# Optimization experiments

Measured on AMD Instinct MI355X. Metric: run time of the kernel, lower is better.

The kernel has to match this reference:

```python
import jax, jax.numpy as jnp
import numpy as np

EMBED_DIM = 1024
EPS = 1e-6


def setup_inputs() -> dict:
    key = jax.random.key(0)
    ks = jax.random.split(key, 9)
    L, B, E = 2048, 4, EMBED_DIM
    s = 1.0 / np.sqrt(E)
    return {
        "query": jax.random.normal(ks[0], (L, B, E), jnp.float32),
        "key": jax.random.normal(ks[1], (L, B, E), jnp.float32),
        "value": jax.random.normal(ks[2], (L, B, E), jnp.float32),
        "Wq": jax.random.normal(ks[3], (E, E), jnp.float32) * s,
        "bq": jnp.zeros((E,), jnp.float32),
        "Wk": jax.random.normal(ks[4], (E, E), jnp.float32) * s,
        "bk": jnp.zeros((E,), jnp.float32),
        "Wv": jax.random.normal(ks[5], (E, E), jnp.float32) * s,
        "bv": jnp.zeros((E,), jnp.float32),
    }


def reference(query, key, value, Wq, bq, Wk, bk, Wv, bv):
    # query: (L, B, E); key/value: (S, B, E)
    L, B, E = query.shape
    S = key.shape[0]
    m = max(L, S)  # static

    # projections + relu feature map, then (B, T, E) layout
    q = jax.nn.relu(jnp.einsum("lbe,fe->lbf", query, Wq) + bq).transpose(1, 0, 2)
    k = jax.nn.relu(jnp.einsum("sbe,fe->sbf", key, Wk) + bk).transpose(1, 0, 2)
    v = (jnp.einsum("sbe,fe->sbf", value, Wv) + bv).transpose(1, 0, 2)

    # cosFormer positional weights: (pi/2) * (i+1) / m, i in [0, T)
    half_pi = jnp.float32(np.pi / 2)
    q_idx = (half_pi * jnp.arange(1, L + 1, dtype=jnp.float32) / m)[None, :, None]
    k_idx = (half_pi * jnp.arange(1, S + 1, dtype=jnp.float32) / m)[None, :, None]

    q_ = jnp.concatenate([q * jnp.sin(q_idx), q * jnp.cos(q_idx)], axis=-1)  # (B, L, 2E)
    k_ = jnp.concatenate([k * jnp.sin(k_idx), k * jnp.cos(k_idx)], axis=-1)  # (B, S, 2E)

    # linear attention: kv_ state (B, E, 2E), normalizer z_ (B, L)
    kv_ = jnp.einsum("nsd,nsm->nmd", k_, v)
    z_ = 1.0 / jnp.maximum(jnp.einsum("nld,nd->nl", q_, k_.sum(axis=1)), EPS)
    attn = jnp.einsum("nld,nmd,nl->nlm", q_, kv_, z_)  # (B, L, E)
    return attn.transpose(1, 0, 2)  # (L, B, E)
```

## Files before the change

kernel.cpp:

```cpp
#include <hip/hip_runtime.h>
#include <hip/hip_fp16.h>


typedef _Float16 f16;
typedef f16 f16x8 __attribute__((ext_vector_type(8)));
typedef f16 f16x4 __attribute__((ext_vector_type(4)));
typedef float f32x4 __attribute__((ext_vector_type(4)));

#define AS1 __attribute__((address_space(1)))
#define AS3 __attribute__((address_space(3)))

__device__ __forceinline__ void gload_lds16(const void* g, void* l) {
  __builtin_amdgcn_global_load_lds((const AS1 void*)g, (AS3 void*)l, 16, 0, 0);
}

__device__ __forceinline__ void xcd_swz(int& bx, int& by, int& bz) {
  const int nx = gridDim.x, ny = gridDim.y;
  const int p = blockIdx.x + nx * (blockIdx.y + ny * blockIdx.z);
  const int chunk = (nx * ny * gridDim.z) >> 3;
  const int l = (p & 7) * chunk + (p >> 3);
  bx = l % nx;
  by = (l / nx) % ny;
  bz = l / (nx * ny);
}

__global__ void cvt3(const float* __restrict__ s0, const float* __restrict__ s1,
                     const float* __restrict__ s2, f16* __restrict__ d0,
                     f16* __restrict__ d1, f16* __restrict__ d2, int n4) {
  const int z = blockIdx.z;
  const float* s = (z == 0) ? s0 : (z == 1) ? s1 : s2;
  f16* d = (z == 0) ? d0 : (z == 1) ? d1 : d2;
  const int i = blockIdx.x * 256 + threadIdx.x;
  if (i >= n4) return;
  const float4 v = ((const float4*)s)[i];
  f16x4 o = { (f16)v.x, (f16)v.y, (f16)v.z, (f16)v.w };
  ((f16x4*)d)[i] = o;
}

__device__ __forceinline__ void mm_core(const f16* __restrict__ A, int lda,
                                        const f16* __restrict__ B, int ldb,
                                        int K, int m0, int n0,
                                        f16* As0, f16* Bs0, f16* As1, f16* Bs1,
                                        f16* As2, f16* Bs2, f16* As3, f16* Bs3,
                                        f32x4 (&acc)[4][4]) {
  const int tid  = threadIdx.x;
  const int lane = tid & 63;
  const int w    = tid >> 6;
  const int wm   = w >> 1, wn = w & 1;
  const int l15  = lane & 15;
  const int quad = lane >> 4;

  const f16* pa0 = A + (long)(m0 + w * 16 + l15) * lda + quad * 8;
  const f16* pa1 = A + (long)(m0 + (8 + w) * 16 + l15) * lda + quad * 8;
  const f16* pb0 = B + (long)(n0 + w * 16 + l15) * ldb + quad * 8;
  int koff = 0;

#define STAGE_(Ab, Bb) do {                        \
    gload_lds16(pa0 + koff, (Ab) + w * 512);       \
    gload_lds16(pa1 + koff, (Ab) + (8 + w) * 512); \
    gload_lds16(pb0 + koff, (Bb) + w * 512);       \
    koff += 32; } while (0)

#define COMPUTE_(Ab, Bb) do {                                                    \
    f16x8 af[4], bf[4];                                                          \
    _Pragma("unroll")                                                            \
    for (int i = 0; i < 4; ++i)                                                  \
      af[i] = *(const f16x8*)((Ab) + (wm * 4 + i) * 512 + lane * 8);             \
    _Pragma("unroll")                                                            \
    for (int j = 0; j < 4; ++j)                                                  \
      bf[j] = *(const f16x8*)((Bb) + (wn * 4 + j) * 512 + lane * 8);             \
    _Pragma("unroll")                                                            \
    for (int i = 0; i < 4; ++i)                                                  \
      _Pragma("unroll")                                                          \
      for (int j = 0; j < 4; ++j)                                                \
        acc[i][j] = __builtin_amdgcn_mfma_f32_16x16x32_f16(af[i], bf[j],         \
                                                           acc[i][j], 0, 0, 0); \
  } while (0)

#define WV3_ asm volatile("s_waitcnt vmcnt(3)" ::: "memory")
#define WV0_ asm volatile("s_waitcnt vmcnt(0)" ::: "memory")
#define BARR_ do { __builtin_amdgcn_s_barrier(); __builtin_amdgcn_sched_barrier(0); } while (0)

  STAGE_(As0, Bs0);
  STAGE_(As1, Bs1);

  const int nt = K >> 5;
  for (int t = 0; t + 5 < nt; t += 4) {
    WV3_; BARR_; STAGE_(As2, Bs2); COMPUTE_(As0, Bs0);
    WV3_; BARR_; STAGE_(As3, Bs3); COMPUTE_(As1, Bs1);
    WV3_; BARR_; STAGE_(As0, Bs0); COMPUTE_(As2, Bs2);
    WV3_; BARR_; STAGE_(As1, Bs1); COMPUTE_(As3, Bs3);
  }
  WV3_; BARR_; STAGE_(As2, Bs2); COMPUTE_(As0, Bs0);
  WV3_; BARR_; STAGE_(As3, Bs3); COMPUTE_(As1, Bs1);
  WV3_; BARR_; COMPUTE_(As2, Bs2);
  WV0_; BARR_; COMPUTE_(As3, Bs3);

#undef STAGE_
#undef COMPUTE_
#undef WV3_
#undef WV0_
#undef BARR_
}

#define GEMM_LDS                                   \
  __shared__ alignas(16) f16 As0[8192];            \
  __shared__ alignas(16) f16 Bs0[4096];            \
  __shared__ alignas(16) f16 As1[8192];            \
  __shared__ alignas(16) f16 Bs1[4096];            \
  __shared__ alignas(16) f16 As2[8192];            \
  __shared__ alignas(16) f16 Bs2[4096];            \
  __shared__ alignas(16) f16 As3[8192];            \
  __shared__ alignas(16) f16 Bs3[4096];

__launch_bounds__(512, 2)
__global__ void proj_gemm(const f16* __restrict__ q16, const f16* __restrict__ k16,
                          const f16* __restrict__ v16, const f16* __restrict__ wq,
                          const f16* __restrict__ wk, const f16* __restrict__ wv,
                          const float* __restrict__ bq, const float* __restrict__ bk,
                          const float* __restrict__ bv,
                          f16* __restrict__ Qf, f16* __restrict__ Kn, f16* __restrict__ Vp) {
  GEMM_LDS
  int bx, by, z;
  xcd_swz(bx, by, z);
  const f16* A = (z == 0) ? q16 : (z == 1) ? k16 : v16;
  const f16* B = (z == 0) ? wq : (z == 1) ? wk : wv;
  const float* bias = (z == 0) ? bq : (z == 1) ? bk : bv;
  const int m0 = by * 256;
  const int n0 = bx * 128;

  f32x4 acc[4][4] = {};
  mm_core(A, 1024, B, 1024, 1024, m0, n0,
          As0, Bs0, As1, Bs1, As2, Bs2, As3, Bs3, acc);

  const int tid  = threadIdx.x;
  const int lane = tid & 63;
  const int w    = tid >> 6;
  const int wm   = w >> 1, wn = w & 1;
  const int l15  = lane & 15;
  const int quad = lane >> 4;

  if (z < 2) {
    f16* C = (z == 0) ? Qf : Kn;
    const int ldc = 2048, halfw = 1024;
#pragma unroll
    for (int i = 0; i < 4; ++i) {
      const int mg = m0 + wm * 64 + i * 16 + quad * 4;
      float sn[4], cn[4];
#pragma unroll
      for (int rr = 0; rr < 4; ++rr) {
        const int l = (mg + rr) >> 2;
        const float ang = 7.6699039394282066e-4f * (float)(l + 1);
        __sincosf(ang, &sn[rr], &cn[rr]);
      }
#pragma unroll
      for (int j = 0; j < 4; ++j) {
        const int ng = n0 + wn * 64 + j * 16 + l15;
        const float bc = bias[ng];
#pragma unroll
        for (int rr = 0; rr < 4; ++rr) {
          const float v = fmaxf(acc[i][j][rr] + bc, 0.f);
          C[(long)(mg + rr) * ldc + ng]         = (f16)(v * sn[rr]);
          C[(long)(mg + rr) * ldc + ng + halfw] = (f16)(v * cn[rr]);
        }
      }
    }
  } else {
    f16* C = Vp;
    const int ldc = 1024;
#pragma unroll
    for (int i = 0; i < 4; ++i) {
      const int mg = m0 + wm * 64 + i * 16 + quad * 4;
#pragma unroll
      for (int j = 0; j < 4; ++j) {
        const int ng = n0 + wn * 64 + j * 16 + l15;
        const float bc = bias[ng];
#pragma unroll
        for (int rr = 0; rr < 4; ++rr)
          C[(long)(mg + rr) * ldc + ng] = (f16)(acc[i][j][rr] + bc);
      }
    }
  }
}

template<int MODE>
__launch_bounds__(512, 2)
__global__ void gemm_bt(const f16* __restrict__ A, int lda,
                        const f16* __restrict__ B, int ldb,
                        void* __restrict__ Cout, int K, int ldc,
                        const float* __restrict__ zvec,
                        long abatch, long bbatch, long cbatch)
{
  GEMM_LDS
  int bx, by, bz;
  xcd_swz(bx, by, bz);
  A += (long)bz * abatch;
  B += (long)bz * bbatch;
  const int m0 = by * 256;
  const int n0 = bx * 128;

  f32x4 acc[4][4] = {};
  mm_core(A, lda, B, ldb, K, m0, n0,
          As0, Bs0, As1, Bs1, As2, Bs2, As3, Bs3, acc);

  const int tid  = threadIdx.x;
  const int lane = tid & 63;
  const int w    = tid >> 6;
  const int wm   = w >> 1, wn = w & 1;
  const int l15  = lane & 15;
  const int quad = lane >> 4;

  if constexpr (MODE == 2) {
    f16* C = (f16*)Cout + (long)bz * cbatch;
#pragma unroll
    for (int i = 0; i < 4; ++i) {
      const int mg = m0 + wm * 64 + i * 16 + quad * 4;
#pragma unroll
      for (int j = 0; j < 4; ++j) {
        const int ng = n0 + wn * 64 + j * 16 + l15;
#pragma unroll
        for (int rr = 0; rr < 4; ++rr)
          C[(long)(mg + rr) * ldc + ng] = (f16)acc[i][j][rr];
      }
    }
  } else {
    float* C = (float*)Cout + (long)bz * cbatch;
#pragma unroll
    for (int i = 0; i < 4; ++i) {
      const int mg = m0 + wm * 64 + i * 16 + quad * 4;
      float zr[4];
#pragma unroll
      for (int rr = 0; rr < 4; ++rr) zr[rr] = zvec[(long)(mg + rr) * 4 + bz];
#pragma unroll
      for (int j = 0; j < 4; ++j) {
        const int ng = n0 + wn * 64 + j * 16 + l15;
#pragma unroll
        for (int rr = 0; rr < 4; ++rr)
          C[(long)(mg + rr) * ldc + ng] = acc[i][j][rr] * zr[rr];
      }
    }
  }
}

__global__ void transpose_fused(const f16* __restrict__ Kn, f16* __restrict__ Kt,
                                const f16* __restrict__ Vp, f16* __restrict__ Vt) {
  __shared__ f16 tile[64 * 72];
  const int z = blockIdx.z;
  const f16* in;
  f16* out;
  long in_batch, out_batch;
  int ldin, ldout, b;
  if (z < 4) {
    in = Kn; out = Kt; in_batch = 2048; out_batch = 2048L * 2048;
    ldin = 8192; ldout = 2048; b = z;
  } else {
    if (blockIdx.x >= 16) return;
    in = Vp; out = Vt; in_batch = 1024; out_batch = 1024L * 2048;
    ldin = 4096; ldout = 2048; b = z - 4;
  }
  in  += (long)b * in_batch;
  out += (long)b * out_batch;
  const int r0 = blockIdx.y * 64;
  const int c0 = blockIdx.x * 64;
  const int t  = threadIdx.x;
  {
    const int r = t >> 2, cs = (t & 3) * 16;
    const f16* src = in + (long)(r0 + r) * ldin + c0 + cs;
    f16x8 v0 = *(const f16x8*)(src);
    f16x8 v1 = *(const f16x8*)(src + 8);
    *(f16x8*)(tile + r * 72 + cs)     = v0;
    *(f16x8*)(tile + r * 72 + cs + 8) = v1;
  }
  __syncthreads();
  {
    const int c = t >> 2, rs = (t & 3) * 16;
    alignas(16) f16 tmp[16];
#pragma unroll
    for (int j = 0; j < 16; ++j) tmp[j] = tile[(rs + j) * 72 + c];
    f16* dst = out + (long)(c0 + c) * ldout + r0 + rs;
    *(f16x8*)(dst)     = *(const f16x8*)(tmp);
    *(f16x8*)(dst + 8) = *(const f16x8*)(tmp + 8);
  }
}

__global__ void ksum_kernel(const f16* __restrict__ Kt, float* __restrict__ ks) {
  const long row = blockIdx.x;
  const int t = threadIdx.x;
  f16x8 v = *(const f16x8*)(Kt + row * 2048 + t * 8);
  float s = 0.f;
#pragma unroll
  for (int j = 0; j < 8; ++j) s += (float)v[j];
#pragma unroll
  for (int off = 32; off > 0; off >>= 1) s += __shfl_down(s, off, 64);
  __shared__ float red[4];
  if ((t & 63) == 0) red[t >> 6] = s;
  __syncthreads();
  if (t == 0) ks[row] = red[0] + red[1] + red[2] + red[3];
}

__global__ void z_kernel(const f16* __restrict__ Qf, const float* __restrict__ ks,
                         float* __restrict__ zb) {
  const long r = blockIdx.x;
  const int t = threadIdx.x;
  const int b = (int)(r & 3);
  f16x8 q = *(const f16x8*)(Qf + r * 2048 + t * 8);
  const float* kp = ks + b * 2048 + t * 8;
  float s = 0.f;
#pragma unroll
  for (int j = 0; j < 8; ++j) s += (float)q[j] * kp[j];
#pragma unroll
  for (int off = 32; off > 0; off >>= 1) s += __shfl_down(s, off, 64);
  __shared__ float red[4];
  if ((t & 63) == 0) red[t >> 6] = s;
  __syncthreads();
  if (t == 0) zb[r] = 1.f / fmaxf(red[0] + red[1] + red[2] + red[3], 1e-6f);
}

extern "C" void kernel_launch(void* const* d_in, const int* in_sizes, int n_in,
                              void* d_out, int out_size, void* d_ws, size_t ws_size,
                              hipStream_t stream) {
  const float* query = (const float*)d_in[0];
  const float* key_  = (const float*)d_in[1];
  const float* value = (const float*)d_in[2];
  const float* Wq    = (const float*)d_in[3];
  const float* bq    = (const float*)d_in[4];
  const float* Wk    = (const float*)d_in[5];
  const float* bk    = (const float*)d_in[6];
  const float* Wv    = (const float*)d_in[7];
  const float* bv    = (const float*)d_in[8];

  char* ws = (char*)d_ws;
  const size_t MB = 1ull << 20;
  f16* wq16 = (f16*)(ws + 0 * MB);
  f16* wk16 = (f16*)(ws + 2 * MB);
  f16* wv16 = (f16*)(ws + 4 * MB);
  f16* q16  = (f16*)(ws + 6 * MB);
  f16* k16  = (f16*)(ws + 22 * MB);
  f16* v16  = (f16*)(ws + 38 * MB);
  f16* Qf   = (f16*)(ws + 54 * MB);
  f16* Kn   = (f16*)(ws + 86 * MB);
  f16* Vp   = (f16*)(ws + 118 * MB);
  f16* Kt   = (f16*)(ws + 6 * MB);
  f16* Vt   = (f16*)(ws + 38 * MB);
  f16* kvb  = (f16*)(ws + 86 * MB);
  float* ks = (float*)(ws + 102 * MB);
  float* zb = (float*)(ws + 103 * MB);

  cvt3<<<dim3(8192, 1, 3), 256, 0, stream>>>(query, key_, value, q16, k16, v16, 2097152);
  cvt3<<<dim3(1024, 1, 3), 256, 0, stream>>>(Wq, Wk, Wv, wq16, wk16, wv16, 262144);

  proj_gemm<<<dim3(8, 32, 3), 512, 0, stream>>>(q16, k16, v16, wq16, wk16, wv16,
                                                bq, bk, bv, Qf, Kn, Vp);

  transpose_fused<<<dim3(32, 32, 8), 256, 0, stream>>>(Kn, Kt, Vp, Vt);

  ksum_kernel<<<8192, 256, 0, stream>>>(Kt, ks);
  z_kernel<<<8192, 256, 0, stream>>>(Qf, ks, zb);

  gemm_bt<2><<<dim3(16, 4, 4), 512, 0, stream>>>(Vt, 2048, Kt, 2048, kvb, 2048, 2048,
                                                 nullptr, 1024L * 2048, 2048L * 2048, 1024L * 2048);
  gemm_bt<3><<<dim3(8, 8, 4), 512, 0, stream>>>(Qf, 8192, kvb, 2048, d_out, 2048, 4096,
                                                zb, 2048, 1024L * 2048, 1024);
}
```

Before: 372.7 us.

## Rewrite projection GEMM with 256x256 tiles and quadrant-interleaved LDS pipeline

The projection GEMM now uses its own main loop with 256x256 output tiles instead of 256x128. The K step is 64, LDS is double-buffered (two 64 KB pairs), and loads are staged in four quarter-tile phases that interleave with MFMA work on the other quadrants. Each block does twice the work and reads each A and B tile once per larger output region, which cuts global and LDS traffic per FLOP. The cost is 128 accumulator registers per lane and 128 KB of LDS per block, which likely limits occupancy to one block per CU despite the launch bound of two, and halves the grid to 384 blocks.

Measured after the change: 379.2 us. Within noise of the previous version (+1.7%).

```diff
diff --git a/kernel.cpp b/kernel.cpp
--- a/kernel.cpp
+++ b/kernel.cpp
@@ -37,12 +37,173 @@
   ((f16x4*)d)[i] = o;
 }
 
-__device__ __forceinline__ void mm_core(const f16* __restrict__ A, int lda,
-                                        const f16* __restrict__ B, int ldb,
-                                        int K, int m0, int n0,
-                                        f16* As0, f16* Bs0, f16* As1, f16* Bs1,
-                                        f16* As2, f16* Bs2, f16* As3, f16* Bs3,
-                                        f32x4 (&acc)[4][4]) {
+__launch_bounds__(512, 2)
+__global__ void proj_gemm(const f16* __restrict__ q16, const f16* __restrict__ k16,
+                          const f16* __restrict__ v16, const f16* __restrict__ wq,
+                          const f16* __restrict__ wk, const f16* __restrict__ wv,
+                          const float* __restrict__ bq, const float* __restrict__ bk,
+                          const float* __restrict__ bv,
+                          f16* __restrict__ Qf, f16* __restrict__ Kn, f16* __restrict__ Vp) {
+  __shared__ alignas(16) f16 As0[16384];
+  __shared__ alignas(16) f16 Bs0[16384];
+  __shared__ alignas(16) f16 As1[16384];
+  __shared__ alignas(16) f16 Bs1[16384];
+
+  int bx, by, z;
+  xcd_swz(bx, by, z);
+  const f16* A = (z == 0) ? q16 : (z == 1) ? k16 : v16;
+  const f16* B = (z == 0) ? wq : (z == 1) ? wk : wv;
+  const float* bias = (z == 0) ? bq : (z == 1) ? bk : bv;
+  const int m0 = by * 256;
+  const int n0 = bx * 256;
+
+  const int tid  = threadIdx.x;
+  const int lane = tid & 63;
+  const int w    = tid >> 6;
+  const int wm   = w >> 2;
+  const int wn   = w & 3;
+  const int l15  = lane & 15;
+  const int quad = lane >> 4;
+  const int lda = 1024, ldb = 1024, K = 1024;
+
+  const f16* gA0 = A + (long)(m0 + w * 16 + l15) * lda + quad * 8;
+  const f16* gA1 = gA0 + 128 * lda;
+  const f16* gB0 = B + (long)(n0 + w * 16 + l15) * ldb + quad * 8;
+  const f16* gB1 = gB0 + 128 * ldb;
+  int ko = 0;
+
+  f32x4 acc[4][4][2] = {};
+  f16x8 af[4][2], bf[2][2];
+
+#define ST_AH0(AW) do { gload_lds16(gA0 + ko, (AW) + w * 1024); \
+                        gload_lds16(gA0 + ko + 32, (AW) + w * 1024 + 512); } while (0)
+#define ST_AH1(AW) do { gload_lds16(gA1 + ko, (AW) + (8 + w) * 1024); \
+                        gload_lds16(gA1 + ko + 32, (AW) + (8 + w) * 1024 + 512); } while (0)
+#define ST_BH0(BW) do { gload_lds16(gB0 + ko, (BW) + w * 1024); \
+                        gload_lds16(gB0 + ko + 32, (BW) + w * 1024 + 512); } while (0)
+#define ST_BH1(BW) do { gload_lds16(gB1 + ko, (BW) + (8 + w) * 1024); \
+                        gload_lds16(gB1 + ko + 32, (BW) + (8 + w) * 1024 + 512); } while (0)
+
+#define RD_AF(AR, qm) do { _Pragma("unroll") \
+    for (int mi = 0; mi < 4; ++mi) { _Pragma("unroll") \
+      for (int kt = 0; kt < 2; ++kt) \
+        af[mi][kt] = *(const f16x8*)((AR) + (((qm) * 8 + wm * 4 + mi) * 2 + kt) * 512 + lane * 8); } } while (0)
+#define RD_BF(BR, qn) do { _Pragma("unroll") \
+    for (int nj = 0; nj < 2; ++nj) { _Pragma("unroll") \
+      for (int kt = 0; kt < 2; ++kt) \
+        bf[nj][kt] = *(const f16x8*)((BR) + (((qn) * 8 + wn * 2 + nj) * 2 + kt) * 512 + lane * 8); } } while (0)
+
+#define MF16(q) do { __builtin_amdgcn_s_setprio(1); _Pragma("unroll") \
+    for (int mi = 0; mi < 4; ++mi) { _Pragma("unroll") \
+      for (int nj = 0; nj < 2; ++nj) { _Pragma("unroll") \
+        for (int kt = 0; kt < 2; ++kt) \
+          acc[q][mi][nj] = __builtin_amdgcn_mfma_f32_16x16x32_f16(af[mi][kt], bf[nj][kt], acc[q][mi][nj], 0, 0, 0); } } \
+    __builtin_amdgcn_s_setprio(0); } while (0)
+
+#define WV4_ asm volatile("s_waitcnt vmcnt(4)" ::: "memory")
+#define WV2_ asm volatile("s_waitcnt vmcnt(2)" ::: "memory")
+#define WV0_ asm volatile("s_waitcnt vmcnt(0)" ::: "memory")
+#define BARR_ do { __builtin_amdgcn_s_barrier(); __builtin_amdgcn_sched_barrier(0); } while (0)
+
+#define TILE(AR, BR, AW, BW) do {                                  \
+    WV4_; BARR_; ST_AH0(AW); RD_AF(AR, 0); RD_BF(BR, 0); MF16(0);  \
+    WV4_; BARR_; ST_BH0(BW); RD_BF(BR, 1); MF16(1);                \
+    WV4_; BARR_; ST_BH1(BW); RD_AF(AR, 1); MF16(2);                \
+          BARR_; ST_AH1(AW); RD_BF(BR, 0); MF16(3);                \
+    ko += 64; } while (0)
+
+#define TILE_LAST(AR, BR) do {                                     \
+    WV4_; BARR_; RD_AF(AR, 0); RD_BF(BR, 0); MF16(0);              \
+    WV2_; BARR_; RD_BF(BR, 1); MF16(1);                            \
+    WV0_; BARR_; RD_AF(AR, 1); MF16(2);                            \
+          BARR_; RD_BF(BR, 0); MF16(3); } while (0)
+
+  ST_AH0(As0); ST_BH0(Bs0); ST_BH1(Bs0); ST_AH1(As0);
+  ko = 64;
+
+  const int nt = K >> 6;
+  for (int t = 0; t + 2 < nt; t += 2) {
+    TILE(As0, Bs0, As1, Bs1);
+    TILE(As1, Bs1, As0, Bs0);
+  }
+  TILE(As0, Bs0, As1, Bs1);
+  TILE_LAST(As1, Bs1);
+
+#undef ST_AH0
+#undef ST_AH1
+#undef ST_BH0
+#undef ST_BH1
+#undef RD_AF
+#undef RD_BF
+#undef MF16
+#undef WV4_
+#undef WV2_
+#undef WV0_
+#undef BARR_
+#undef TILE
+#undef TILE_LAST
+
+  const int QM[4] = {0, 0, 1, 1};
+  const int QN[4] = {0, 1, 1, 0};
+  if (z < 2) {
+    f16* C = (z == 0) ? Qf : Kn;
+    const int ldc = 2048, halfw = 1024;
+#pragma unroll
+    for (int q = 0; q < 4; ++q) {
+      const int rbase = m0 + QM[q] * 128 + wm * 64;
+      const int cbase = n0 + QN[q] * 128 + wn * 32;
+#pragma unroll
+      for (int mi = 0; mi < 4; ++mi) {
+        const int mg = rbase + mi * 16 + quad * 4;
+        float sn[4], cn[4];
+#pragma unroll
+        for (int rr = 0; rr < 4; ++rr) {
+          const int l = (mg + rr) >> 2;
+          const float ang = 7.6699039394282066e-4f * (float)(l + 1);
+          __sincosf(ang, &sn[rr], &cn[rr]);
+        }
+#pragma unroll
+        for (int nj = 0; nj < 2; ++nj) {
+          const int ng = cbase + nj * 16 + l15;
+          const float bc = bias[ng];
+#pragma unroll
+          for (int rr = 0; rr < 4; ++rr) {
+            const float v = fmaxf(acc[q][mi][nj][rr] + bc, 0.f);
+            C[(long)(mg + rr) * ldc + ng]         = (f16)(v * sn[rr]);
+            C[(long)(mg + rr) * ldc + ng + halfw] = (f16)(v * cn[rr]);
+          }
+        }
+      }
+    }
+  } else {
+    f16* C = Vp;
+    const int ldc = 1024;
+#pragma unroll
+    for (int q = 0; q < 4; ++q) {
+      const int rbase = m0 + QM[q] * 128 + wm * 64;
+      const int cbase = n0 + QN[q] * 128 + wn * 32;
+#pragma unroll
+      for (int mi = 0; mi < 4; ++mi) {
+        const int mg = rbase + mi * 16 + quad * 4;
+#pragma unroll
+        for (int nj = 0; nj < 2; ++nj) {
+          const int ng = cbase + nj * 16 + l15;
+          const float bc = bias[ng];
+#pragma unroll
+          for (int rr = 0; rr < 4; ++rr)
+            C[(long)(mg + rr) * ldc + ng] = (f16)(acc[q][mi][nj][rr] + bc);
+        }
+      }
+    }
+  }
+}
+
+__device__ __forceinline__ void mm_core_kva(const f16* __restrict__ A, int lda,
+                                            const f16* __restrict__ B, int ldb,
+                                            int K, int m0, int n0,
+                                            f16* As0, f16* Bs0, f16* As1, f16* Bs1,
+                                            f16* As2, f16* Bs2, f16* As3, f16* Bs3,
+                                            f32x4 (&acc)[4][4]) {
   const int tid  = threadIdx.x;
   const int lane = tid & 63;
   const int w    = tid >> 6;
@@ -113,76 +274,6 @@
   __shared__ alignas(16) f16 As3[8192];            \
   __shared__ alignas(16) f16 Bs3[4096];
 
-__launch_bounds__(512, 2)
-__global__ void proj_gemm(const f16* __restrict__ q16, const f16* __restrict__ k16,
-                          const f16* __restrict__ v16, const f16* __restrict__ wq,
-                          const f16* __restrict__ wk, const f16* __restrict__ wv,
-                          const float* __restrict__ bq, const float* __restrict__ bk,
-                          const float* __restrict__ bv,
-                          f16* __restrict__ Qf, f16* __restrict__ Kn, f16* __restrict__ Vp) {
-  GEMM_LDS
-  int bx, by, z;
-  xcd_swz(bx, by, z);
-  const f16* A = (z == 0) ? q16 : (z == 1) ? k16 : v16;
-  const f16* B = (z == 0) ? wq : (z == 1) ? wk : wv;
-  const float* bias = (z == 0) ? bq : (z == 1) ? bk : bv;
-  const int m0 = by * 256;
-  const int n0 = bx * 128;
-
-  f32x4 acc[4][4] = {};
-  mm_core(A, 1024, B, 1024, 1024, m0, n0,
-          As0, Bs0, As1, Bs1, As2, Bs2, As3, Bs3, acc);
-
-  const int tid  = threadIdx.x;
-  const int lane = tid & 63;
-  const int w    = tid >> 6;
-  const int wm   = w >> 1, wn = w & 1;
-  const int l15  = lane & 15;
-  const int quad = lane >> 4;
-
-  if (z < 2) {
-    f16* C = (z == 0) ? Qf : Kn;
-    const int ldc = 2048, halfw = 1024;
-#pragma unroll
-    for (int i = 0; i < 4; ++i) {
-      const int mg = m0 + wm * 64 + i * 16 + quad * 4;
-      float sn[4], cn[4];
-#pragma unroll
-      for (int rr = 0; rr < 4; ++rr) {
-        const int l = (mg + rr) >> 2;
-        const float ang = 7.6699039394282066e-4f * (float)(l + 1);
-        __sincosf(ang, &sn[rr], &cn[rr]);
-      }
-#pragma unroll
-      for (int j = 0; j < 4; ++j) {
-        const int ng = n0 + wn * 64 + j * 16 + l15;
-        const float bc = bias[ng];
-#pragma unroll
-        for (int rr = 0; rr < 4; ++rr) {
-          const float v = fmaxf(acc[i][j][rr] + bc, 0.f);
-          C[(long)(mg + rr) * ldc + ng]         = (f16)(v * sn[rr]);
-          C[(long)(mg + rr) * ldc + ng + halfw] = (f16)(v * cn[rr]);
-        }
-      }
-    }
-  } else {
-    f16* C = Vp;
-    const int ldc = 1024;
-#pragma unroll
-    for (int i = 0; i < 4; ++i) {
-      const int mg = m0 + wm * 64 + i * 16 + quad * 4;
-#pragma unroll
-      for (int j = 0; j < 4; ++j) {
-        const int ng = n0 + wn * 64 + j * 16 + l15;
-        const float bc = bias[ng];
-#pragma unroll
-        for (int rr = 0; rr < 4; ++rr)
-          C[(long)(mg + rr) * ldc + ng] = (f16)(acc[i][j][rr] + bc);
-      }
-    }
-  }
-}
-
 template<int MODE>
 __launch_bounds__(512, 2)
 __global__ void gemm_bt(const f16* __restrict__ A, int lda,
@@ -200,8 +291,8 @@
   const int n0 = bx * 128;
 
   f32x4 acc[4][4] = {};
-  mm_core(A, lda, B, ldb, K, m0, n0,
-          As0, Bs0, As1, Bs1, As2, Bs2, As3, Bs3, acc);
+  mm_core_kva(A, lda, B, ldb, K, m0, n0,
+              As0, Bs0, As1, Bs1, As2, Bs2, As3, Bs3, acc);
 
   const int tid  = threadIdx.x;
   const int lane = tid & 63;
@@ -349,7 +440,7 @@
   cvt3<<<dim3(8192, 1, 3), 256, 0, stream>>>(query, key_, value, q16, k16, v16, 2097152);
   cvt3<<<dim3(1024, 1, 3), 256, 0, stream>>>(Wq, Wk, Wv, wq16, wk16, wv16, 262144);
 
-  proj_gemm<<<dim3(8, 32, 3), 512, 0, stream>>>(q16, k16, v16, wq16, wk16, wv16,
+  proj_gemm<<<dim3(4, 32, 3), 512, 0, stream>>>(q16, k16, v16, wq16, wk16, wv16,
                                                 bq, bk, bv, Qf, Kn, Vp);
 
   transpose_fused<<<dim3(32, 32, 8), 256, 0, stream>>>(Kn, Kt, Vp, Vt);
```
